# Optimization experiments

Measured on AMD Instinct MI355X. Metric: run time of the kernel, lower is better.

Reference implementation:

```python
import jax, jax.numpy as jnp
import numpy as np

N = 40000      # nodes
E = 640000     # edges (avg degree 16)
IN = 128       # in_dim
H = 8          # n_heads
D = 16         # out_dim per head
ED = 64        # edge_dim
C = H * D      # out_channel = 128 == IN -> residual is Identity
EPS = 1e-5


def setup_inputs() -> dict:
    key = jax.random.key(0)
    ks = jax.random.split(key, 20)

    def lin(k, shape):
        fan_in = shape[-1]
        return jax.random.normal(k, shape, dtype=jnp.float32) / np.sqrt(fan_in)

    return {
        "q": jax.random.normal(ks[0], (N, IN), dtype=jnp.float32),
        "k": jax.random.normal(ks[1], (N, IN), dtype=jnp.float32),
        "v": jax.random.normal(ks[2], (N, IN), dtype=jnp.float32),
        "edge_feat": jax.random.normal(ks[3], (E, ED), dtype=jnp.float32),
        "src": jax.random.randint(ks[4], (E,), 0, N, dtype=jnp.int32),
        "dst": jax.random.randint(ks[5], (E,), 0, N, dtype=jnp.int32),
        "Wq": lin(ks[6], (C, IN)),
        "Wk": lin(ks[7], (C, IN)),
        "Wv": lin(ks[8], (C, IN)),
        "We": lin(ks[9], (H, ED)),
        "be": jnp.zeros((H,), dtype=jnp.float32),
        "Wo": lin(ks[10], (C, C)),
        "W1": lin(ks[11], (2 * C, C)),
        "b1": jnp.zeros((2 * C,), dtype=jnp.float32),
        "W2": lin(ks[12], (C, 2 * C)),
        "b2": jnp.zeros((C,), dtype=jnp.float32),
        "g1": jnp.ones((C,), dtype=jnp.float32),
        "bt1": jnp.zeros((C,), dtype=jnp.float32),
        "g2": jnp.ones((C,), dtype=jnp.float32),
        "bt2": jnp.zeros((C,), dtype=jnp.float32),
    }


def _batch_norm(x, g, b):
    mu = x.mean(axis=0)
    var = x.var(axis=0)  # biased, matching torch BN normalization
    return (x - mu) * jax.lax.rsqrt(var + EPS) * g + b


def reference(q, k, v, edge_feat, src, dst, Wq, Wk, Wv, We, be, Wo,
              W1, b1, W2, b2, g1, bt1, g2, bt2):
    n = q.shape[0]
    qd = (q @ Wq.T).reshape(n, H, D)        # [N,H,D] dst queries
    ksrc = (k @ Wk.T).reshape(-1, H, D)     # [N,H,D]
    vsrc = (v @ Wv.T).reshape(-1, H, D)     # [N,H,D]

    # per-edge attention scores: v_dot_u(q_dst, k_src) / sqrt(D)
    scores = jnp.einsum('ehd,ehd->eh', qd[dst], ksrc[src]) / jnp.sqrt(jnp.float32(D))
    # edge_mode == 'ADD': add per-head edge bias
    scores = scores + edge_feat @ We.T + be  # [E,H]

    # edge softmax normalized by destination node (segment softmax)
    smax = jax.ops.segment_max(scores, dst, num_segments=n)      # [N,H]
    ex = jnp.exp(scores - smax[dst])
    denom = jax.ops.segment_sum(ex, dst, num_segments=n)         # [N,H]
    attn = ex / denom[dst]                                       # [E,H]

    # scatter-weighted aggregation: sum_e attn * v_src -> dst
    agg = jax.ops.segment_sum(attn[:, :, None] * vsrc[src], dst, num_segments=n)  # [N,H,D]

    rst = agg.reshape(n, C) @ Wo.T
    rst = rst + q                    # residual (Identity: in_dim == out_channel)
    rst = _batch_norm(rst, g1, bt1)

    h = jnp.maximum(rst @ W1.T + b1, 0.0) @ W2.T + b2  # FFN
    rst = _batch_norm(h + rst, g2, bt2)
    return rst
```

## Files before the change

### kernel.cpp

```cpp
#include <hip/hip_runtime.h>
#include <cstdint>
#include <cstddef>

#define Nn 40000
#define Ne 640000
#define CC 128
#define EPSbn 1e-5f

typedef __attribute__((ext_vector_type(8))) __bf16 bf16x8;
typedef __attribute__((ext_vector_type(4))) float floatx4;

__device__ inline unsigned short f2bf(float x){
  union { float f; unsigned u; } c; c.f = x;
  unsigned r = c.u + 0x7fffu + ((c.u >> 16) & 1u);
  return (unsigned short)(r >> 16);
}
__device__ inline float bflo(unsigned u){ return __uint_as_float(u << 16); }
__device__ inline float bfhi(unsigned u){ return __uint_as_float(u & 0xffff0000u); }

__global__ void zero_k(int* __restrict__ p, int n){
  int i = blockIdx.x*blockDim.x + threadIdx.x;
  if (i < n) p[i] = 0;
}

template<int KTILES,bool ABF16,bool HASBIAS,bool HASRES,bool RELU,bool AFFA,bool AFFRES,bool OUTB16>
__global__ __launch_bounds__(256,2) void mgemm_k(
    const void* __restrict__ Ap, const float* __restrict__ W,
    const float* __restrict__ bias, const float* __restrict__ res,
    const float* __restrict__ sc, const float* __restrict__ sh,
    void* __restrict__ Cp, int M, int Ncols)
{
  constexpr int K = KTILES * 128;
  __shared__ __align__(16) unsigned short As[128*136];
  __shared__ __align__(16) unsigned short Ws[128*136];
  const int tid  = threadIdx.x;
  const int lane = tid & 63;
  const int wv   = tid >> 6;
  const int m    = lane & 15;
  const int quad = lane >> 4;
  const int row0 = blockIdx.x * 128;
  const int col0 = blockIdx.y * 128;
  floatx4 acc[2][8] = {};

  for (int kt = 0; kt < K; kt += 128) {
    #pragma unroll 4
    for (int it = 0; it < 16; ++it) {
      int s = tid + it*256;
      int r = s >> 5;
      int c = (s & 31) << 2;
      int gr = row0 + r; if (gr >= M) gr = M - 1;
      ushort4 ua;
      if (ABF16) {
        ua = *(const ushort4*)((const unsigned short*)Ap + (size_t)gr*K + kt + c);
      } else {
        float4 a4 = *(const float4*)((const float*)Ap + (size_t)gr*K + kt + c);
        if (AFFA) {
          int kk = kt + c;
          a4.x = a4.x*sc[kk  ] + sh[kk  ];
          a4.y = a4.y*sc[kk+1] + sh[kk+1];
          a4.z = a4.z*sc[kk+2] + sh[kk+2];
          a4.w = a4.w*sc[kk+3] + sh[kk+3];
        }
        ua.x = f2bf(a4.x); ua.y = f2bf(a4.y); ua.z = f2bf(a4.z); ua.w = f2bf(a4.w);
      }
      *(ushort4*)&As[r*136 + c] = ua;
      float4 w4 = *(const float4*)(W + (size_t)(col0 + r)*K + kt + c);
      ushort4 uw;
      uw.x = f2bf(w4.x); uw.y = f2bf(w4.y); uw.z = f2bf(w4.z); uw.w = f2bf(w4.w);
      *(ushort4*)&Ws[r*136 + c] = uw;
    }
    __syncthreads();
    #pragma unroll
    for (int ks = 0; ks < 4; ++ks) {
      int ko = ks*32 + quad*8;
      bf16x8 a0 = *(const bf16x8*)&As[(32*wv      + m)*136 + ko];
      bf16x8 a1 = *(const bf16x8*)&As[(32*wv + 16 + m)*136 + ko];
      #pragma unroll
      for (int j = 0; j < 8; ++j) {
        bf16x8 bj = *(const bf16x8*)&Ws[(16*j + m)*136 + ko];
        acc[0][j] = __builtin_amdgcn_mfma_f32_16x16x32_bf16(a0, bj, acc[0][j], 0, 0, 0);
        acc[1][j] = __builtin_amdgcn_mfma_f32_16x16x32_bf16(a1, bj, acc[1][j], 0, 0, 0);
      }
    }
    __syncthreads();
  }

  float bcol[8], scv[8], shv[8];
  #pragma unroll
  for (int j = 0; j < 8; ++j) {
    int gcol = col0 + 16*j + m;
    if (HASBIAS) bcol[j] = bias[gcol];
    if (AFFRES) { scv[j] = sc[gcol]; shv[j] = sh[gcol]; }
  }
  #pragma unroll
  for (int rt = 0; rt < 2; ++rt) {
    #pragma unroll
    for (int rg = 0; rg < 4; ++rg) {
      int grow = row0 + 32*wv + 16*rt + quad*4 + rg;
      if (grow < M) {
        #pragma unroll
        for (int j = 0; j < 8; ++j) {
          int gcol = col0 + 16*j + m;
          float o = acc[rt][j][rg];
          if (HASBIAS) o += bcol[j];
          if (HASRES) {
            float rr = res[(size_t)grow*Ncols + gcol];
            if (AFFRES) rr = rr*scv[j] + shv[j];
            o += rr;
          }
          if (RELU) o = fmaxf(o, 0.f);
          if (OUTB16) ((unsigned short*)Cp)[(size_t)grow*Ncols + gcol] = f2bf(o);
          else        ((float*)Cp)[(size_t)grow*Ncols + gcol] = o;
        }
      }
    }
  }
}

__global__ __launch_bounds__(256) void ebias_k(
    const float* __restrict__ ef, const float* __restrict__ We,
    const float* __restrict__ be, const int* __restrict__ pos,
    unsigned short* __restrict__ EBs)
{
  __shared__ float efs[32][68];
  __shared__ float Wes[8][68];
  __shared__ float bes[8];
  int tid = threadIdx.x;
  if (tid < 8) bes[tid] = be[tid];
  for (int i = tid; i < 512; i += 256) Wes[i>>6][i&63] = We[i];
  int e0 = blockIdx.x * 32;
  #pragma unroll
  for (int l = 0; l < 2; ++l) {
    int idx = tid + l*256;
    int r   = idx >> 4;
    int q4  = (idx & 15) << 2;
    float4 t = *(const float4*)(ef + (size_t)(e0 + r)*64 + q4);
    efs[r][q4]=t.x; efs[r][q4+1]=t.y; efs[r][q4+2]=t.z; efs[r][q4+3]=t.w;
  }
  __syncthreads();
  int h = tid & 7, el = tid >> 3;
  int e = e0 + el;
  float es = 0.f;
  #pragma unroll
  for (int kk = 0; kk < 64; kk += 4) {
    float4 a = *(const float4*)&efs[el][kk];
    float4 b = *(const float4*)&Wes[h][kk];
    es += a.x*b.x + a.y*b.y + a.z*b.z + a.w*b.w;
  }
  EBs[(size_t)pos[e]*8 + h] = f2bf(es + bes[h]);
}

__global__ void hist_k(const int* __restrict__ dst, int* __restrict__ counts, int E){
  int i = blockIdx.x*blockDim.x + threadIdx.x;
  if (i < E) atomicAdd(&counts[dst[i]], 1);
}

__global__ __launch_bounds__(256) void scan1_k(
    const int* __restrict__ counts, int* __restrict__ part,
    int* __restrict__ bsums, int n)
{
  int tid = threadIdx.x;
  int base = blockIdx.x*1024 + tid*4;
  int v0 = (base   < n) ? counts[base  ] : 0;
  int v1 = (base+1 < n) ? counts[base+1] : 0;
  int v2 = (base+2 < n) ? counts[base+2] : 0;
  int v3 = (base+3 < n) ? counts[base+3] : 0;
  int t1 = v0+v1, t2 = t1+v2, t3 = t2+v3;
  int lane = tid & 63, wv = tid >> 6;
  int x = t3;
  #pragma unroll
  for (int off = 1; off < 64; off <<= 1) {
    int y = __shfl_up(x, off);
    if (lane >= off) x += y;
  }
  __shared__ int wt[4];
  if (lane == 63) wt[wv] = x;
  __syncthreads();
  int wbase = 0;
  #pragma unroll
  for (int w = 0; w < 4; ++w) if (w < wv) wbase += wt[w];
  int excl = wbase + x - t3;
  if (base   < n) part[base  ] = excl;
  if (base+1 < n) part[base+1] = excl + v0;
  if (base+2 < n) part[base+2] = excl + t1;
  if (base+3 < n) part[base+3] = excl + t2;
  if (tid == 255) bsums[blockIdx.x] = wbase + x;
}

__global__ void scan2_k(int* bsums, int nb){
  int lane = threadIdx.x;
  int v = (lane < nb) ? bsums[lane] : 0;
  int x = v;
  #pragma unroll
  for (int off = 1; off < 64; off <<= 1) {
    int y = __shfl_up(x, off);
    if (lane >= off) x += y;
  }
  if (lane < nb) bsums[lane] = x - v;
}

__global__ void scan3_k(int* __restrict__ offsets, const int* __restrict__ bsums,
                        int* __restrict__ cursor, int n, int E){
  int i = blockIdx.x*blockDim.x + threadIdx.x;
  if (i < n) {
    int o = offsets[i] + bsums[i >> 10];
    offsets[i] = o;
    cursor[i]  = o;
  }
  if (i == 0) offsets[n] = E;
}

__global__ void scatter_k(const int* __restrict__ dst, const int* __restrict__ src,
                          int* __restrict__ cursor, int* __restrict__ pos,
                          int* __restrict__ srcs, int E){
  int i = blockIdx.x*blockDim.x + threadIdx.x;
  if (i < E) {
    int p = atomicAdd(&cursor[dst[i]], 1);
    pos[i]  = p;
    srcs[p] = src[i];
  }
}

__global__ __launch_bounds__(256) void agg_k(
    const unsigned* __restrict__ QDb, const unsigned* __restrict__ KSb,
    const unsigned* __restrict__ VSb, const unsigned short* __restrict__ EBs,
    const int* __restrict__ offsets, const int* __restrict__ srcs,
    float* __restrict__ agg, int n)
{
  int wv = threadIdx.x >> 6, lane = threadIdx.x & 63;
  int node = blockIdx.x*4 + wv;
  if (node >= n) return;
  unsigned qt = QDb[(size_t)node*64 + lane];
  float q0 = bflo(qt) * 0.25f;
  float q1 = bfhi(qt) * 0.25f;
  int beg = offsets[node], end = offsets[node+1];
  int hoff = lane >> 3;
  float acc0 = 0.f, acc1 = 0.f, den = 0.f;
  for (int base = beg; base < end; base += 64) {
    int mrem = end - base; if (mrem > 64) mrem = 64;
    int ss = (lane < mrem) ? srcs[base + lane] : 0;
    int j = 0;
    for (; j + 2 <= mrem; j += 2) {
      int s0 = __shfl(ss, j);
      int s1 = __shfl(ss, j+1);
      unsigned kt0 = KSb[(size_t)s0*64 + lane];
      unsigned kt1 = KSb[(size_t)s1*64 + lane];
      unsigned vt0 = VSb[(size_t)s0*64 + lane];
      unsigned vt1 = VSb[(size_t)s1*64 + lane];
      float p0 = q0*bflo(kt0) + q1*bfhi(kt0);
      float p1 = q0*bflo(kt1) + q1*bfhi(kt1);
      p0 += __shfl_xor(p0, 1);  p1 += __shfl_xor(p1, 1);
      p0 += __shfl_xor(p0, 2);  p1 += __shfl_xor(p1, 2);
      p0 += __shfl_xor(p0, 4);  p1 += __shfl_xor(p1, 4);
      float eb0 = bflo((unsigned)EBs[(size_t)(base+j  )*8 + hoff] << 16 >> 16 << 16);
      float eb1 = bflo((unsigned)EBs[(size_t)(base+j+1)*8 + hoff] << 16 >> 16 << 16);
      eb0 = __uint_as_float(((unsigned)EBs[(size_t)(base+j  )*8 + hoff]) << 16);
      eb1 = __uint_as_float(((unsigned)EBs[(size_t)(base+j+1)*8 + hoff]) << 16);
      float w0 = __expf(p0 + eb0);
      float w1 = __expf(p1 + eb1);
      acc0 += w0*bflo(vt0) + w1*bflo(vt1);
      acc1 += w0*bfhi(vt0) + w1*bfhi(vt1);
      den  += w0 + w1;
    }
    if (j < mrem) {
      int s0 = __shfl(ss, j);
      unsigned kt0 = KSb[(size_t)s0*64 + lane];
      unsigned vt0 = VSb[(size_t)s0*64 + lane];
      float p0 = q0*bflo(kt0) + q1*bfhi(kt0);
      p0 += __shfl_xor(p0, 1);
      p0 += __shfl_xor(p0, 2);
      p0 += __shfl_xor(p0, 4);
      float eb0 = __uint_as_float(((unsigned)EBs[(size_t)(base+j)*8 + hoff]) << 16);
      float w0 = __expf(p0 + eb0);
      acc0 += w0*bflo(vt0);
      acc1 += w0*bfhi(vt0);
      den  += w0;
    }
  }
  float inv = den > 0.f ? 1.f/den : 0.f;
  float2 o; o.x = acc0*inv; o.y = acc1*inv;
  *(float2*)(agg + (size_t)node*128 + 2*lane) = o;
}

__global__ __launch_bounds__(256) void bnstats_k(const float* __restrict__ X,
    float* __restrict__ sum, float* __restrict__ sumsq, int M)
{
  int col  = threadIdx.x & 127;
  int half = threadIdx.x >> 7;
  float s = 0.f, q = 0.f;
  for (int r = blockIdx.x*2 + half; r < M; r += gridDim.x*2) {
    float v = X[(size_t)r*128 + col];
    s += v; q += v*v;
  }
  __shared__ float ls[256], lq[256];
  ls[threadIdx.x] = s; lq[threadIdx.x] = q;
  __syncthreads();
  if (half == 0) {
    atomicAdd(&sum[col],   s + ls[threadIdx.x + 128]);
    atomicAdd(&sumsq[col], q + lq[threadIdx.x + 128]);
  }
}

__global__ void bnfin_k(const float* sum, const float* sq, const float* g,
                        const float* bt, float* scale, float* shift, int M){
  int c = threadIdx.x;
  float mu  = sum[c] / (float)M;
  float var = sq[c] / (float)M - mu*mu;
  float s = g[c] * rsqrtf(var + EPSbn);
  scale[c] = s;
  shift[c] = bt[c] - mu*s;
}

__global__ void bnapply_k(const float* __restrict__ Y, const float* __restrict__ scale,
                          const float* __restrict__ shift, float* __restrict__ out, int total){
  int n4 = total >> 2;
  for (int i = blockIdx.x*blockDim.x + threadIdx.x; i < n4; i += gridDim.x*blockDim.x) {
    float4 vv = ((const float4*)Y)[i];
    int c = (i << 2) & 127;
    vv.x = vv.x*scale[c  ] + shift[c  ];
    vv.y = vv.y*scale[c+1] + shift[c+1];
    vv.z = vv.z*scale[c+2] + shift[c+2];
    vv.w = vv.w*scale[c+3] + shift[c+3];
    ((float4*)out)[i] = vv;
  }
}

extern "C" void kernel_launch(void* const* d_in, const int* in_sizes, int n_in,
                              void* d_out, int out_size, void* d_ws, size_t ws_size,
                              hipStream_t stream) {
  const float* q   = (const float*)d_in[0];
  const float* k   = (const float*)d_in[1];
  const float* v   = (const float*)d_in[2];
  const float* ef  = (const float*)d_in[3];
  const int*   src = (const int*)d_in[4];
  const int*   dst = (const int*)d_in[5];
  const float* Wq  = (const float*)d_in[6];
  const float* Wk  = (const float*)d_in[7];
  const float* Wv  = (const float*)d_in[8];
  const float* We  = (const float*)d_in[9];
  const float* be  = (const float*)d_in[10];
  const float* Wo  = (const float*)d_in[11];
  const float* W1  = (const float*)d_in[12];
  const float* b1  = (const float*)d_in[13];
  const float* W2  = (const float*)d_in[14];
  const float* b2  = (const float*)d_in[15];
  const float* g1  = (const float*)d_in[16];
  const float* bt1 = (const float*)d_in[17];
  const float* g2  = (const float*)d_in[18];
  const float* bt2 = (const float*)d_in[19];
  float* out = (float*)d_out;

  float* ws = (float*)d_ws;
  const size_t NB = (size_t)Nn * CC;
  float* QDb = ws;
  float* KSb = ws + NB/2;
  float* VSb = ws + NB;
  unsigned short* EBs = (unsigned short*)(ws + 3*NB/2);
  float* AGG = ws + 2*NB;
  float* RST = ws + 3*NB;
  float* H1  = ws;
  float* Y   = AGG;
  float* bn = ws + 4*NB;
  float* sum1 = bn;       float* sq1 = bn+128;  float* sc1 = bn+256; float* sh1 = bn+384;
  float* sum2 = bn+512;   float* sq2 = bn+640;  float* sc2 = bn+768; float* sh2 = bn+896;
  int* ib      = (int*)(bn + 1024);
  int* counts  = ib;
  int* offsets = ib + 40000;
  int* cursor  = ib + 80001;
  int* posA    = ib + 120001;
  int* srcsA   = ib + 760001;
  int* bsums   = ib + 1400001;

  zero_k<<<dim3(157), 256, 0, stream>>>(counts, Nn);
  zero_k<<<dim3(4),   256, 0, stream>>>((int*)bn, 1024);

  hist_k<<<dim3(2500), 256, 0, stream>>>(dst, counts, Ne);
  scan1_k<<<dim3(40), 256, 0, stream>>>(counts, offsets, bsums, Nn);
  scan2_k<<<dim3(1), 64, 0, stream>>>(bsums, 40);
  scan3_k<<<dim3(157), 256, 0, stream>>>(offsets, bsums, cursor, Nn, Ne);
  scatter_k<<<dim3(2500), 256, 0, stream>>>(dst, src, cursor, posA, srcsA, Ne);

  dim3 g1d(313, 1);
  mgemm_k<1,false,false,false,false,false,false,true><<<g1d,256,0,stream>>>(q, Wq, nullptr, nullptr, nullptr, nullptr, QDb, Nn, 128);
  mgemm_k<1,false,false,false,false,false,false,true><<<g1d,256,0,stream>>>(k, Wk, nullptr, nullptr, nullptr, nullptr, KSb, Nn, 128);
  mgemm_k<1,false,false,false,false,false,false,true><<<g1d,256,0,stream>>>(v, Wv, nullptr, nullptr, nullptr, nullptr, VSb, Nn, 128);

  ebias_k<<<dim3(Ne/32), 256, 0, stream>>>(ef, We, be, posA, EBs);

  agg_k<<<dim3(Nn/4), 256, 0, stream>>>((const unsigned*)QDb, (const unsigned*)KSb,
                                        (const unsigned*)VSb, EBs,
                                        offsets, srcsA, AGG, Nn);

  mgemm_k<1,false,false,true,false,false,false,false><<<g1d,256,0,stream>>>(AGG, Wo, nullptr, q, nullptr, nullptr, RST, Nn, 128);

  bnstats_k<<<dim3(256), 256, 0, stream>>>(RST, sum1, sq1, Nn);
  bnfin_k<<<dim3(1), 128, 0, stream>>>(sum1, sq1, g1, bt1, sc1, sh1, Nn);

  mgemm_k<1,false,true,false,true,true,false,true><<<dim3(313,2),256,0,stream>>>(RST, W1, b1, nullptr, sc1, sh1, H1, Nn, 256);

  mgemm_k<2,true,true,true,false,false,true,false><<<g1d,256,0,stream>>>(H1, W2, b2, RST, sc1, sh1, Y, Nn, 128);

  bnstats_k<<<dim3(256), 256, 0, stream>>>(Y, sum2, sq2, Nn);
  bnfin_k<<<dim3(1), 128, 0, stream>>>(sum2, sq2, g2, bt2, sc2, sh2, Nn);
  bnapply_k<<<dim3(1024), 256, 0, stream>>>(Y, sc2, sh2, out, Nn*CC);
}
```

Baseline: 571.6 us.

## Fuse BN stats into GEMM epilogues, batch QKV GEMMs, interleave K/V for gathers

Launches the Q/K/V projections as one 3-slice grid and writes K and V into an interleaved bf16 layout so the aggregation kernel fetches both with a single 8-byte gather per edge. The aggregation loop is unrolled to four edges for more memory-level parallelism. Batch-norm column sums and sums of squares are computed in the GEMM epilogues with shuffle/shared reductions and atomics, removing two standalone statistics passes over the activations. The zeroing launches are merged; atomics per block and more registers in the GEMM epilogue are the trade-off.

```diff
diff --git a/kernel.cpp b/kernel.cpp
--- a/kernel.cpp
+++ b/kernel.cpp
@@ -23,16 +23,29 @@
   if (i < n) p[i] = 0;
 }
 
-template<int KTILES,bool ABF16,bool HASBIAS,bool HASRES,bool RELU,bool AFFA,bool AFFRES,bool OUTB16>
+struct GA3 {
+  const void* A0; const void* A1; const void* A2;
+  const float* W0; const float* W1; const float* W2;
+  void* C0; void* C1; void* C2;
+  int m0, m1, m2;
+};
+
+template<int KTILES,bool ABF16,bool HASBIAS,bool HASRES,bool RELU,bool AFFA,bool AFFRES,bool BNSTAT>
 __global__ __launch_bounds__(256,2) void mgemm_k(
-    const void* __restrict__ Ap, const float* __restrict__ W,
-    const float* __restrict__ bias, const float* __restrict__ res,
+    GA3 ga, const float* __restrict__ bias, const float* __restrict__ res,
     const float* __restrict__ sc, const float* __restrict__ sh,
-    void* __restrict__ Cp, int M, int Ncols)
+    float* __restrict__ bnS, float* __restrict__ bnQ,
+    int M, int Ncols)
 {
   constexpr int K = KTILES * 128;
   __shared__ __align__(16) unsigned short As[128*136];
   __shared__ __align__(16) unsigned short Ws[128*136];
+  const int z = blockIdx.z;
+  const void*  Ap = (z==0) ? ga.A0 : (z==1) ? ga.A1 : ga.A2;
+  const float* W  = (z==0) ? ga.W0 : (z==1) ? ga.W1 : ga.W2;
+  void*        Cp = (z==0) ? ga.C0 : (z==1) ? ga.C1 : ga.C2;
+  const int mode  = (z==0) ? ga.m0 : (z==1) ? ga.m1 : ga.m2;
+
   const int tid  = threadIdx.x;
   const int lane = tid & 63;
   const int wv   = tid >> 6;
@@ -92,6 +105,7 @@
     if (HASBIAS) bcol[j] = bias[gcol];
     if (AFFRES) { scv[j] = sc[gcol]; shv[j] = sh[gcol]; }
   }
+  float ps[8] = {}, pq[8] = {};
   #pragma unroll
   for (int rt = 0; rt < 2; ++rt) {
     #pragma unroll
@@ -109,9 +123,36 @@
             o += rr;
           }
           if (RELU) o = fmaxf(o, 0.f);
-          if (OUTB16) ((unsigned short*)Cp)[(size_t)grow*Ncols + gcol] = f2bf(o);
-          else        ((float*)Cp)[(size_t)grow*Ncols + gcol] = o;
+          if (BNSTAT) { ps[j] += o; pq[j] += o*o; }
+          if (mode == 0)      ((float*)Cp)[(size_t)grow*Ncols + gcol] = o;
+          else if (mode == 1) ((unsigned short*)Cp)[(size_t)grow*Ncols + gcol] = f2bf(o);
+          else {
+            int ph = mode - 2;
+            *(unsigned short*)((char*)Cp + (size_t)grow*512 + (gcol>>1)*8 + ph*4 + (gcol&1)*2) = f2bf(o);
+          }
         }
+      }
+    }
+  }
+  if (BNSTAT) {
+    float* sS = (float*)&As[0];
+    float* sQ = sS + 4*128;
+    #pragma unroll
+    for (int j = 0; j < 8; ++j) {
+      float s = ps[j], qq = pq[j];
+      s += __shfl_xor(s, 16); qq += __shfl_xor(qq, 16);
+      s += __shfl_xor(s, 32); qq += __shfl_xor(qq, 32);
+      if (quad == 0) { sS[wv*128 + 16*j + m] = s; sQ[wv*128 + 16*j + m] = qq; }
+    }
+    __syncthreads();
+    if (wv == 0) {
+      #pragma unroll
+      for (int c = 0; c < 128; c += 64) {
+        int cc = c + lane;
+        float s  = sS[cc] + sS[128+cc] + sS[256+cc] + sS[384+cc];
+        float qq = sQ[cc] + sQ[128+cc] + sQ[256+cc] + sQ[384+cc];
+        atomicAdd(&bnS[col0 + cc], s);
+        atomicAdd(&bnQ[col0 + cc], qq);
       }
     }
   }
@@ -222,8 +263,8 @@
 }
 
 __global__ __launch_bounds__(256) void agg_k(
-    const unsigned* __restrict__ QDb, const unsigned* __restrict__ KSb,
-    const unsigned* __restrict__ VSb, const unsigned short* __restrict__ EBs,
+    const unsigned* __restrict__ QDb, const uint2* __restrict__ KV,
+    const unsigned short* __restrict__ EBs,
     const int* __restrict__ offsets, const int* __restrict__ srcs,
     float* __restrict__ agg, int n)
 {
@@ -240,65 +281,51 @@
     int mrem = end - base; if (mrem > 64) mrem = 64;
     int ss = (lane < mrem) ? srcs[base + lane] : 0;
     int j = 0;
-    for (; j + 2 <= mrem; j += 2) {
+    for (; j + 4 <= mrem; j += 4) {
       int s0 = __shfl(ss, j);
       int s1 = __shfl(ss, j+1);
-      unsigned kt0 = KSb[(size_t)s0*64 + lane];
-      unsigned kt1 = KSb[(size_t)s1*64 + lane];
-      unsigned vt0 = VSb[(size_t)s0*64 + lane];
-      unsigned vt1 = VSb[(size_t)s1*64 + lane];
-      float p0 = q0*bflo(kt0) + q1*bfhi(kt0);
-      float p1 = q0*bflo(kt1) + q1*bfhi(kt1);
-      p0 += __shfl_xor(p0, 1);  p1 += __shfl_xor(p1, 1);
-      p0 += __shfl_xor(p0, 2);  p1 += __shfl_xor(p1, 2);
-      p0 += __shfl_xor(p0, 4);  p1 += __shfl_xor(p1, 4);
-      float eb0 = bflo((unsigned)EBs[(size_t)(base+j  )*8 + hoff] << 16 >> 16 << 16);
-      float eb1 = bflo((unsigned)EBs[(size_t)(base+j+1)*8 + hoff] << 16 >> 16 << 16);
-      eb0 = __uint_as_float(((unsigned)EBs[(size_t)(base+j  )*8 + hoff]) << 16);
-      eb1 = __uint_as_float(((unsigned)EBs[(size_t)(base+j+1)*8 + hoff]) << 16);
+      int s2 = __shfl(ss, j+2);
+      int s3 = __shfl(ss, j+3);
+      uint2 kv0 = KV[(size_t)s0*64 + lane];
+      uint2 kv1 = KV[(size_t)s1*64 + lane];
+      uint2 kv2 = KV[(size_t)s2*64 + lane];
+      uint2 kv3 = KV[(size_t)s3*64 + lane];
+      float p0 = q0*bflo(kv0.x) + q1*bfhi(kv0.x);
+      float p1 = q0*bflo(kv1.x) + q1*bfhi(kv1.x);
+      float p2 = q0*bflo(kv2.x) + q1*bfhi(kv2.x);
+      float p3 = q0*bflo(kv3.x) + q1*bfhi(kv3.x);
+      p0 += __shfl_xor(p0, 1); p1 += __shfl_xor(p1, 1); p2 += __shfl_xor(p2, 1); p3 += __shfl_xor(p3, 1);
+      p0 += __shfl_xor(p0, 2); p1 += __shfl_xor(p1, 2); p2 += __shfl_xor(p2, 2); p3 += __shfl_xor(p3, 2);
+      p0 += __shfl_xor(p0, 4); p1 += __shfl_xor(p1, 4); p2 += __shfl_xor(p2, 4); p3 += __shfl_xor(p3, 4);
+      float eb0 = __uint_as_float(((unsigned)EBs[(size_t)(base+j  )*8 + hoff]) << 16);
+      float eb1 = __uint_as_float(((unsigned)EBs[(size_t)(base+j+1)*8 + hoff]) << 16);
+      float eb2 = __uint_as_float(((unsigned)EBs[(size_t)(base+j+2)*8 + hoff]) << 16);
+      float eb3 = __uint_as_float(((unsigned)EBs[(size_t)(base+j+3)*8 + hoff]) << 16);
       float w0 = __expf(p0 + eb0);
       float w1 = __expf(p1 + eb1);
-      acc0 += w0*bflo(vt0) + w1*bflo(vt1);
-      acc1 += w0*bfhi(vt0) + w1*bfhi(vt1);
-      den  += w0 + w1;
-    }
-    if (j < mrem) {
+      float w2 = __expf(p2 + eb2);
+      float w3 = __expf(p3 + eb3);
+      acc0 += w0*bflo(kv0.y) + w1*bflo(kv1.y) + w2*bflo(kv2.y) + w3*bflo(kv3.y);
+      acc1 += w0*bfhi(kv0.y) + w1*bfhi(kv1.y) + w2*bfhi(kv2.y) + w3*bfhi(kv3.y);
+      den  += (w0 + w1) + (w2 + w3);
+    }
+    for (; j < mrem; ++j) {
       int s0 = __shfl(ss, j);
-      unsigned kt0 = KSb[(size_t)s0*64 + lane];
-      unsigned vt0 = VSb[(size_t)s0*64 + lane];
-      float p0 = q0*bflo(kt0) + q1*bfhi(kt0);
+      uint2 kv0 = KV[(size_t)s0*64 + lane];
+      float p0 = q0*bflo(kv0.x) + q1*bfhi(kv0.x);
       p0 += __shfl_xor(p0, 1);
       p0 += __shfl_xor(p0, 2);
       p0 += __shfl_xor(p0, 4);
       float eb0 = __uint_as_float(((unsigned)EBs[(size_t)(base+j)*8 + hoff]) << 16);
       float w0 = __expf(p0 + eb0);
-      acc0 += w0*bflo(vt0);
-      acc1 += w0*bfhi(vt0);
+      acc0 += w0*bflo(kv0.y);
+      acc1 += w0*bfhi(kv0.y);
       den  += w0;
     }
   }
   float inv = den > 0.f ? 1.f/den : 0.f;
   float2 o; o.x = acc0*inv; o.y = acc1*inv;
   *(float2*)(agg + (size_t)node*128 + 2*lane) = o;
-}
-
-__global__ __launch_bounds__(256) void bnstats_k(const float* __restrict__ X,
-    float* __restrict__ sum, float* __restrict__ sumsq, int M)
-{
-  int col  = threadIdx.x & 127;
-  int half = threadIdx.x >> 7;
-  float s = 0.f, q = 0.f;
-  for (int r = blockIdx.x*2 + half; r < M; r += gridDim.x*2) {
-    float v = X[(size_t)r*128 + col];
-    s += v; q += v*v;
-  }
-  __shared__ float ls[256], lq[256];
-  ls[threadIdx.x] = s; lq[threadIdx.x] = q;
-  __syncthreads();
-  if (half == 0) {
-    atomicAdd(&sum[col],   s + ls[threadIdx.x + 128]);
-    atomicAdd(&sumsq[col], q + lq[threadIdx.x + 128]);
-  }
 }
 
 __global__ void bnfin_k(const float* sum, const float* sq, const float* g,
@@ -353,8 +380,7 @@
   float* ws = (float*)d_ws;
   const size_t NB = (size_t)Nn * CC;
   float* QDb = ws;
-  float* KSb = ws + NB/2;
-  float* VSb = ws + NB;
+  float* KV  = ws + NB/2;
   unsigned short* EBs = (unsigned short*)(ws + 3*NB/2);
   float* AGG = ws + 2*NB;
   float* RST = ws + 3*NB;
@@ -371,8 +397,7 @@
   int* srcsA   = ib + 760001;
   int* bsums   = ib + 1400001;
 
-  zero_k<<<dim3(157), 256, 0, stream>>>(counts, Nn);
-  zero_k<<<dim3(4),   256, 0, stream>>>((int*)bn, 1024);
+  zero_k<<<dim3(161), 256, 0, stream>>>((int*)bn, 1024 + Nn);
 
   hist_k<<<dim3(2500), 256, 0, stream>>>(dst, counts, Ne);
   scan1_k<<<dim3(40), 256, 0, stream>>>(counts, offsets, bsums, Nn);
@@ -380,27 +405,42 @@
   scan3_k<<<dim3(157), 256, 0, stream>>>(offsets, bsums, cursor, Nn, Ne);
   scatter_k<<<dim3(2500), 256, 0, stream>>>(dst, src, cursor, posA, srcsA, Ne);
 
-  dim3 g1d(313, 1);
-  mgemm_k<1,false,false,false,false,false,false,true><<<g1d,256,0,stream>>>(q, Wq, nullptr, nullptr, nullptr, nullptr, QDb, Nn, 128);
-  mgemm_k<1,false,false,false,false,false,false,true><<<g1d,256,0,stream>>>(k, Wk, nullptr, nullptr, nullptr, nullptr, KSb, Nn, 128);
-  mgemm_k<1,false,false,false,false,false,false,true><<<g1d,256,0,stream>>>(v, Wv, nullptr, nullptr, nullptr, nullptr, VSb, Nn, 128);
+  {
+    GA3 ga;
+    ga.A0 = q;  ga.A1 = k;  ga.A2 = v;
+    ga.W0 = Wq; ga.W1 = Wk; ga.W2 = Wv;
+    ga.C0 = QDb; ga.C1 = KV; ga.C2 = KV;
+    ga.m0 = 1; ga.m1 = 2; ga.m2 = 3;
+    mgemm_k<1,false,false,false,false,false,false,false><<<dim3(313,1,3),256,0,stream>>>(
+        ga, nullptr, nullptr, nullptr, nullptr, nullptr, nullptr, Nn, 128);
+  }
 
   ebias_k<<<dim3(Ne/32), 256, 0, stream>>>(ef, We, be, posA, EBs);
 
-  agg_k<<<dim3(Nn/4), 256, 0, stream>>>((const unsigned*)QDb, (const unsigned*)KSb,
-                                        (const unsigned*)VSb, EBs,
+  agg_k<<<dim3(Nn/4), 256, 0, stream>>>((const unsigned*)QDb, (const uint2*)KV, EBs,
                                         offsets, srcsA, AGG, Nn);
 
-  mgemm_k<1,false,false,true,false,false,false,false><<<g1d,256,0,stream>>>(AGG, Wo, nullptr, q, nullptr, nullptr, RST, Nn, 128);
-
-  bnstats_k<<<dim3(256), 256, 0, stream>>>(RST, sum1, sq1, Nn);
+  {
+    GA3 ga = {};
+    ga.A0 = AGG; ga.W0 = Wo; ga.C0 = RST; ga.m0 = 0;
+    mgemm_k<1,false,false,true,false,false,false,true><<<dim3(313,1,1),256,0,stream>>>(
+        ga, nullptr, q, nullptr, nullptr, sum1, sq1, Nn, 128);
+  }
   bnfin_k<<<dim3(1), 128, 0, stream>>>(sum1, sq1, g1, bt1, sc1, sh1, Nn);
 
-  mgemm_k<1,false,true,false,true,true,false,true><<<dim3(313,2),256,0,stream>>>(RST, W1, b1, nullptr, sc1, sh1, H1, Nn, 256);
-
-  mgemm_k<2,true,true,true,false,false,true,false><<<g1d,256,0,stream>>>(H1, W2, b2, RST, sc1, sh1, Y, Nn, 128);
-
-  bnstats_k<<<dim3(256), 256, 0, stream>>>(Y, sum2, sq2, Nn);
+  {
+    GA3 ga = {};
+    ga.A0 = RST; ga.W0 = W1; ga.C0 = H1; ga.m0 = 1;
+    mgemm_k<1,false,true,false,true,true,false,false><<<dim3(313,2,1),256,0,stream>>>(
+        ga, b1, nullptr, sc1, sh1, nullptr, nullptr, Nn, 256);
+  }
+
+  {
+    GA3 ga = {};
+    ga.A0 = H1; ga.W0 = W2; ga.C0 = Y; ga.m0 = 0;
+    mgemm_k<2,true,true,true,false,false,true,true><<<dim3(313,1,1),256,0,stream>>>(
+        ga, b2, RST, sc1, sh1, sum2, sq2, Nn, 128);
+  }
   bnfin_k<<<dim3(1), 128, 0, stream>>>(sum2, sq2, g2, bt2, sc2, sh2, Nn);
   bnapply_k<<<dim3(1024), 256, 0, stream>>>(Y, sc2, sh2, out, Nn*CC);
 }
```

After: 574.3 us. No clear change (+0.5%).
